# Kernel tuning notes

Measured on AMD Instinct MI355X. Metric: run time of the kernel, lower is better.

The kernel has to match this reference:

```python
import jax, jax.numpy as jnp
import numpy as np

RADIUS = 0.2
NSAMPLE = 32
USE_XYZ = True

B, N, S, C = 8, 8192, 2048, 64


def setup_inputs() -> dict:
    key = jax.random.key(0)
    k1, k2, k3 = jax.random.split(key, 3)
    xyz = jax.random.uniform(k1, (B, N, 3), dtype=jnp.float32)
    new_xyz = jax.random.uniform(k2, (B, S, 3), dtype=jnp.float32)
    features = jax.random.normal(k3, (B, N, C), dtype=jnp.float32)
    return {"xyz": xyz, "new_xyz": new_xyz, "features": features}


def _ball_query(new_xyz, xyz, radius, nsample):
    # new_xyz: (B,S,3), xyz: (B,N,3) -> idx (B,S,nsample) int32
    n = xyz.shape[1]
    d2 = jnp.sum((new_xyz[:, :, None, :] - xyz[:, None, :, :]) ** 2, axis=-1)  # (B,S,N)
    mask = d2 < radius * radius
    # keys: index j if inside ball else N (sentinel); smallest nsample keys = first
    # nsample in-ball indices in ascending j order (matches CUDA ball_query order).
    keys = jnp.where(mask, jnp.arange(n, dtype=jnp.int32), jnp.int32(n))
    neg_vals, _ = jax.lax.top_k(-keys, nsample)  # top_k of -keys -> smallest keys
    idx = -neg_vals  # (B,S,nsample), ascending
    first = idx[..., 0:1]
    idx = jnp.where(idx == n, first, idx)   # pad empty slots with first hit
    idx = jnp.where(idx == n, 0, idx)       # balls with zero hits -> index 0
    return idx


def _group(points, idx):
    # points: (B,N,D), idx: (B,S,K) -> (B,S,K,D)
    return jax.vmap(lambda p, i: p[i])(points, idx)


def reference(xyz, new_xyz, features):
    idx = _ball_query(new_xyz, xyz, RADIUS, NSAMPLE)
    grouped_xyz = _group(xyz, idx) - new_xyz[:, :, None, :]  # (B,S,K,3)
    grouped_feat = _group(features, idx)                      # (B,S,K,C)
    if USE_XYZ:
        new_features = jnp.concatenate([grouped_xyz, grouped_feat], axis=-1)
    else:
        new_features = grouped_feat
    return jnp.transpose(new_features, (0, 3, 1, 2))  # (B, C+3, S, K)
```

## Files before the change

kernel.cpp:

```cpp
#include <hip/hip_runtime.h>

#define BB 8
#define NN 8192
#define SS 2048
#define CC 64
#define NS 32
#define COUT 67
#define QT 8
#define PMAX 35

__global__ __launch_bounds__(256) void scan_kernel(
    const float* __restrict__ xyz,
    const float* __restrict__ new_xyz,
    int* __restrict__ idx_ws)
{
#pragma clang fp contract(off)
    const int wave = threadIdx.x >> 6;
    const int lane = threadIdx.x & 63;
    const int qid  = blockIdx.x * 4 + wave;
    const int b = qid >> 11;
    const int s = qid & 2047;

    const float R2 = 0.04f;

    const float* ctr = new_xyz + ((size_t)b * SS + s) * 3;
    const float cx = ctr[0], cy = ctr[1], cz = ctr[2];
    const float* xb = xyz + (size_t)b * NN * 3;

    int* myidx = idx_ws + (size_t)qid * NS;
    const unsigned long long lt = (1ull << lane) - 1ull;

    int total = 0;
    int firstIdx = -1;
    for (int j0 = 0; j0 < NN && total < NS; j0 += 256) {
        float d2v[4];
#pragma unroll
        for (int u = 0; u < 4; ++u) {
            const int j = j0 + u * 64 + lane;
            const float* p = xb + (size_t)j * 3;
            const float dx = p[0] - cx;
            const float dy = p[1] - cy;
            const float dz = p[2] - cz;
            float d2 = dx * dx;
            d2 = d2 + dy * dy;
            d2 = d2 + dz * dz;
            d2v[u] = d2;
        }
#pragma unroll
        for (int u = 0; u < 4; ++u) {
            const bool hit = d2v[u] < R2;
            const unsigned long long mask = __ballot(hit);
            if (firstIdx < 0 && mask != 0ull)
                firstIdx = j0 + u * 64 + __builtin_ctzll(mask);
            if (hit) {
                const int pos = total + __popcll(mask & lt);
                if (pos < NS) myidx[pos] = j0 + u * 64 + lane;
            }
            total += __popcll(mask);
        }
    }
    if (total < NS) {
        const int fill = (total > 0) ? firstIdx : 0;
        if (lane >= total && lane < NS) myidx[lane] = fill;
    }
}

__global__ __launch_bounds__(256) void gather_kernel(
    const float* __restrict__ xyz,
    const float* __restrict__ new_xyz,
    const float* __restrict__ feat,
    const int* __restrict__ idx_ws,
    float* __restrict__ out)
{
#pragma clang fp contract(off)
    __shared__ float tile[PMAX * QT * NS];
    __shared__ int idx_sh[QT * NS];

    const int t     = threadIdx.x;
    const int sTile = blockIdx.x;
    const int half  = blockIdx.y;
    const int b     = blockIdx.z;

    const int s0 = sTile * QT;
    const int qbase = (b << 11) + s0;

    idx_sh[t] = idx_ws[(size_t)qbase * NS + t];
    __syncthreads();

    const int q = t >> 5;
    const int row = idx_sh[t];

    const float* frow = feat + ((size_t)b * NN + row) * CC + half * 32;
    if (half == 0) {
        const float* ctr = new_xyz + ((size_t)b * SS + s0 + q) * 3;
        const float* p   = xyz + ((size_t)b * NN + row) * 3;
        tile[0 * 256 + t] = p[0] - ctr[0];
        tile[1 * 256 + t] = p[1] - ctr[1];
        tile[2 * 256 + t] = p[2] - ctr[2];
#pragma unroll
        for (int i = 0; i < 8; ++i) {
            const float4 f = *(const float4*)(frow + i * 4);
            tile[(3 + i * 4 + 0) * 256 + t] = f.x;
            tile[(3 + i * 4 + 1) * 256 + t] = f.y;
            tile[(3 + i * 4 + 2) * 256 + t] = f.z;
            tile[(3 + i * 4 + 3) * 256 + t] = f.w;
        }
    } else {
#pragma unroll
        for (int i = 0; i < 8; ++i) {
            const float4 f = *(const float4*)(frow + i * 4);
            tile[(i * 4 + 0) * 256 + t] = f.x;
            tile[(i * 4 + 1) * 256 + t] = f.y;
            tile[(i * 4 + 2) * 256 + t] = f.z;
            tile[(i * 4 + 3) * 256 + t] = f.w;
        }
    }
    __syncthreads();

    const int P     = half ? 32 : PMAX;
    const int cbase = half ? PMAX : 0;
    const int wv = t >> 6;
    const int ln = t & 63;
    const size_t plane = (size_t)SS * NS;
    float* ob = out + (((size_t)b * COUT + cbase) * SS + s0) * NS;
#pragma unroll
    for (int i = 0; i < 9; ++i) {
        const int p = i * 4 + wv;
        if (p < P) {
            const float4 v = *(const float4*)(tile + p * 256 + ln * 4);
            *(float4*)(ob + (size_t)p * plane + ln * 4) = v;
        }
    }
}

extern "C" void kernel_launch(void* const* d_in, const int* in_sizes, int n_in,
                              void* d_out, int out_size, void* d_ws, size_t ws_size,
                              hipStream_t stream) {
    const float* xyz     = (const float*)d_in[0];
    const float* new_xyz = (const float*)d_in[1];
    const float* feat    = (const float*)d_in[2];
    float* out = (float*)d_out;
    int* idx_ws = (int*)d_ws;

    scan_kernel<<<dim3((BB * SS) / 4), dim3(256), 0, stream>>>(xyz, new_xyz, idx_ws);
    gather_kernel<<<dim3(SS / QT, 2, BB), dim3(256), 0, stream>>>(xyz, new_xyz, feat, idx_ws, out);
}
```

Before: 195.2 us.

## Vectorize ball-query point loads and split gather across four channel quarters

```diff
diff --git a/kernel.cpp b/kernel.cpp
--- a/kernel.cpp
+++ b/kernel.cpp
@@ -7,7 +7,7 @@
 #define NS 32
 #define COUT 67
 #define QT 8
-#define PMAX 35
+#define P0 19
 
 __global__ __launch_bounds__(256) void scan_kernel(
     const float* __restrict__ xyz,
@@ -33,31 +33,62 @@
     int total = 0;
     int firstIdx = -1;
     for (int j0 = 0; j0 < NN && total < NS; j0 += 256) {
+        const float4* p4 = (const float4*)(xb + (size_t)(j0 + (lane << 2)) * 3);
+        const float4 A  = p4[0];
+        const float4 Bv = p4[1];
+        const float4 Cv = p4[2];
         float d2v[4];
+        {
+            const float dx = A.x - cx, dy = A.y - cy, dz = A.z - cz;
+            float d2 = dx * dx; d2 = d2 + dy * dy; d2 = d2 + dz * dz;
+            d2v[0] = d2;
+        }
+        {
+            const float dx = A.w - cx, dy = Bv.x - cy, dz = Bv.y - cz;
+            float d2 = dx * dx; d2 = d2 + dy * dy; d2 = d2 + dz * dz;
+            d2v[1] = d2;
+        }
+        {
+            const float dx = Bv.z - cx, dy = Bv.w - cy, dz = Cv.x - cz;
+            float d2 = dx * dx; d2 = d2 + dy * dy; d2 = d2 + dz * dz;
+            d2v[2] = d2;
+        }
+        {
+            const float dx = Cv.y - cx, dy = Cv.z - cy, dz = Cv.w - cz;
+            float d2 = dx * dx; d2 = d2 + dy * dy; d2 = d2 + dz * dz;
+            d2v[3] = d2;
+        }
+
+        unsigned long long M[4];
+#pragma unroll
+        for (int u = 0; u < 4; ++u) M[u] = __ballot(d2v[u] < R2);
+
+        if (firstIdx < 0) {
+            int fmin = 0x7fffffff;
+#pragma unroll
+            for (int u = 0; u < 4; ++u)
+                if (M[u] != 0ull) {
+                    const int j = j0 + (__builtin_ctzll(M[u]) << 2) + u;
+                    fmin = (j < fmin) ? j : fmin;
+                }
+            if (fmin != 0x7fffffff) firstIdx = fmin;
+        }
+
+        int below = 0;
+#pragma unroll
+        for (int u = 0; u < 4; ++u) below += (int)__popcll(M[u] & lt);
+
+        int own = 0;
 #pragma unroll
         for (int u = 0; u < 4; ++u) {
-            const int j = j0 + u * 64 + lane;
-            const float* p = xb + (size_t)j * 3;
-            const float dx = p[0] - cx;
-            const float dy = p[1] - cy;
-            const float dz = p[2] - cz;
-            float d2 = dx * dx;
-            d2 = d2 + dy * dy;
-            d2 = d2 + dz * dz;
-            d2v[u] = d2;
+            if (d2v[u] < R2) {
+                const int pos = total + below + own;
+                if (pos < NS) myidx[pos] = j0 + (lane << 2) + u;
+                ++own;
+            }
         }
 #pragma unroll
-        for (int u = 0; u < 4; ++u) {
-            const bool hit = d2v[u] < R2;
-            const unsigned long long mask = __ballot(hit);
-            if (firstIdx < 0 && mask != 0ull)
-                firstIdx = j0 + u * 64 + __builtin_ctzll(mask);
-            if (hit) {
-                const int pos = total + __popcll(mask & lt);
-                if (pos < NS) myidx[pos] = j0 + u * 64 + lane;
-            }
-            total += __popcll(mask);
-        }
+        for (int u = 0; u < 4; ++u) total += (int)__popcll(M[u]);
     }
     if (total < NS) {
         const int fill = (total > 0) ? firstIdx : 0;
@@ -73,12 +104,12 @@
     float* __restrict__ out)
 {
 #pragma clang fp contract(off)
-    __shared__ float tile[PMAX * QT * NS];
+    __shared__ float tile[P0 * QT * NS];
     __shared__ int idx_sh[QT * NS];
 
     const int t     = threadIdx.x;
     const int sTile = blockIdx.x;
-    const int half  = blockIdx.y;
+    const int quad  = blockIdx.y;
     const int b     = blockIdx.z;
 
     const int s0 = sTile * QT;
@@ -90,41 +121,33 @@
     const int q = t >> 5;
     const int row = idx_sh[t];
 
-    const float* frow = feat + ((size_t)b * NN + row) * CC + half * 32;
-    if (half == 0) {
+    const float* frow = feat + ((size_t)b * NN + row) * CC + quad * 16;
+    const int pb = (quad == 0) ? 3 : 0;
+    if (quad == 0) {
         const float* ctr = new_xyz + ((size_t)b * SS + s0 + q) * 3;
         const float* p   = xyz + ((size_t)b * NN + row) * 3;
         tile[0 * 256 + t] = p[0] - ctr[0];
         tile[1 * 256 + t] = p[1] - ctr[1];
         tile[2 * 256 + t] = p[2] - ctr[2];
+    }
 #pragma unroll
-        for (int i = 0; i < 8; ++i) {
-            const float4 f = *(const float4*)(frow + i * 4);
-            tile[(3 + i * 4 + 0) * 256 + t] = f.x;
-            tile[(3 + i * 4 + 1) * 256 + t] = f.y;
-            tile[(3 + i * 4 + 2) * 256 + t] = f.z;
-            tile[(3 + i * 4 + 3) * 256 + t] = f.w;
-        }
-    } else {
-#pragma unroll
-        for (int i = 0; i < 8; ++i) {
-            const float4 f = *(const float4*)(frow + i * 4);
-            tile[(i * 4 + 0) * 256 + t] = f.x;
-            tile[(i * 4 + 1) * 256 + t] = f.y;
-            tile[(i * 4 + 2) * 256 + t] = f.z;
-            tile[(i * 4 + 3) * 256 + t] = f.w;
-        }
+    for (int i = 0; i < 4; ++i) {
+        const float4 f = *(const float4*)(frow + i * 4);
+        tile[(pb + i * 4 + 0) * 256 + t] = f.x;
+        tile[(pb + i * 4 + 1) * 256 + t] = f.y;
+        tile[(pb + i * 4 + 2) * 256 + t] = f.z;
+        tile[(pb + i * 4 + 3) * 256 + t] = f.w;
     }
     __syncthreads();
 
-    const int P     = half ? 32 : PMAX;
-    const int cbase = half ? PMAX : 0;
+    const int P     = (quad == 0) ? P0 : 16;
+    const int cbase = (quad == 0) ? 0 : (3 + quad * 16);
     const int wv = t >> 6;
     const int ln = t & 63;
     const size_t plane = (size_t)SS * NS;
     float* ob = out + (((size_t)b * COUT + cbase) * SS + s0) * NS;
 #pragma unroll
-    for (int i = 0; i < 9; ++i) {
+    for (int i = 0; i < 5; ++i) {
         const int p = i * 4 + wv;
         if (p < P) {
             const float4 v = *(const float4*)(tile + p * 256 + ln * 4);
@@ -143,5 +166,5 @@
     int* idx_ws = (int*)d_ws;
 
     scan_kernel<<<dim3((BB * SS) / 4), dim3(256), 0, stream>>>(xyz, new_xyz, idx_ws);
-    gather_kernel<<<dim3(SS / QT, 2, BB), dim3(256), 0, stream>>>(xyz, new_xyz, feat, idx_ws, out);
+    gather_kernel<<<dim3(SS / QT, 4, BB), dim3(256), 0, stream>>>(xyz, new_xyz, feat, idx_ws, out);
 }
```

Result: no change. 193.6 us (-0.9%).
